# Optimization experiments

Hardware: AMD Instinct MI355X
Metric: run time of the kernel (lower is better)

## Reference

```python
import jax, jax.numpy as jnp
import numpy as np

B, S, D = 8, 2048, 512
DK, DV = 64, 64

def setup_inputs() -> dict:
    key = jax.random.key(0)
    ks = jax.random.split(key, 9)
    glorot = lambda k, shape: jax.random.uniform(k, shape, jnp.float32, -1.0, 1.0) * np.sqrt(6.0 / (shape[0] + shape[-1] if len(shape) > 1 else shape[0] + 1))
    return {
        "x_q": jax.random.normal(ks[0], (B, S, D), jnp.float32),
        "x_k": jax.random.normal(ks[1], (B, S, D), jnp.float32),
        "x_v": jax.random.normal(ks[2], (B, S, D), jnp.float32),
        "Wq": glorot(ks[3], (D, DK)), "bq": glorot(ks[4], (DK,)),
        "Wk": glorot(ks[5], (D, DK)), "bk": glorot(ks[6], (DK,)),
        "Wv": glorot(ks[7], (D, DV)), "bv": glorot(ks[8], (DV,)),
    }

def reference(x_q, x_k, x_v, Wq, bq, Wk, bk, Wv, bv):
    q = jnp.einsum("bsd,dk->bsk", x_q, Wq) + bq          # [B,S,DK]
    k = jnp.einsum("bsd,dk->bsk", x_k, Wk) + bk          # [B,S,DK]
    v = jnp.einsum("bsd,dv->bsv", x_v, Wv) + bv          # [B,S,DV]
    scale = 1.0 / np.sqrt(DK).astype(np.float32)
    scores = jnp.einsum("bqk,bsk->bqs", q, k) * scale     # [B,S,S]
    attn = jax.nn.softmax(scores, axis=-1)
    return jnp.einsum("bqs,bsv->bqv", attn, v)            # [B,S,DV]
```

## Files before the change

kernel.cpp:

```cpp
#include <hip/hip_runtime.h>
#include <stdint.h>

typedef __bf16 bf16;
typedef __bf16 bf16x8 __attribute__((ext_vector_type(8)));
typedef float f32x4 __attribute__((ext_vector_type(4)));

struct alignas(8) U16x4 { uint16_t v[4]; };

__device__ __forceinline__ f32x4 mfma16(bf16x8 a, bf16x8 b, f32x4 c) {
    return __builtin_amdgcn_mfma_f32_16x16x32_bf16(a, b, c, 0, 0, 0);
}

__device__ __forceinline__ void gload_lds16(const void* g, void* l) {
    __builtin_amdgcn_global_load_lds(
        (const __attribute__((address_space(1))) uint32_t*)g,
        (__attribute__((address_space(3))) uint32_t*)l, 16, 0, 0);
}

__device__ __forceinline__ uint16_t bf_bits(bf16 v) {
    return __builtin_bit_cast(uint16_t, v);
}

__device__ __forceinline__ float bf2f(uint16_t u) {
    uint32_t x = (uint32_t)u << 16;
    return __builtin_bit_cast(float, x);
}

#define QSCALE 0.18033688011112042f

__global__ __launch_bounds__(256)
void wprep_kernel(const float* __restrict__ Wq, const float* __restrict__ Wk,
                  const float* __restrict__ Wv, uint16_t* __restrict__ wt)
{
    const int tid = blockIdx.x * 256 + threadIdx.x;
    const int p   = tid >> 12;
    const int rem = tid & 4095;
    const int kt  = rem >> 8;
    const int f   = (rem >> 6) & 3;
    const int l   = rem & 63;
    const int n   = (l & 15) + 16 * f;
    const int k0  = kt * 32 + (l >> 4) * 8;
    const float* W = (p == 0) ? Wq : (p == 1) ? Wk : Wv;
    bf16x8 v;
    #pragma unroll
    for (int j = 0; j < 8; j++)
        v[j] = (bf16)W[(size_t)(k0 + j) * 64 + n];
    *(bf16x8*)(wt + (size_t)tid * 8) = v;
}

__global__ __launch_bounds__(256, 2)
void proj_kernel(const float* __restrict__ xq, const float* __restrict__ xk,
                 const float* __restrict__ xv,
                 const float* __restrict__ bq, const float* __restrict__ bk,
                 const float* __restrict__ bv,
                 const uint16_t* __restrict__ wt,
                 uint16_t* __restrict__ q_ws, uint16_t* __restrict__ k_ws,
                 uint16_t* __restrict__ vt_ws)
{
    const int p = blockIdx.y;
    const float* x    = (p == 0) ? xq : (p == 1) ? xk : xv;
    const float* bias = (p == 0) ? bq : (p == 1) ? bk : bv;
    const uint16_t* wtp = wt + (size_t)p * 32768;

    const int m0 = blockIdx.x * 64;
    const int t  = threadIdx.x;
    const int l  = t & 63;
    const int w  = t >> 6;

    __shared__ __align__(16) uint16_t sW[32768];

    const int arow = m0 + w * 16 + (l & 15);
    const int kg   = (l >> 4) * 8;
    const float* xrow = x + (size_t)arow * 512 + kg;

    float4 av0[8], av1[8];
    #pragma unroll
    for (int s = 0; s < 8; s++) {
        av0[s] = *(const float4*)(xrow + s * 32);
        av1[s] = *(const float4*)(xrow + s * 32 + 4);
    }

    #pragma unroll
    for (int r = 0; r < 16; r++)
        gload_lds16(wtp + (size_t)(r * 256 + t) * 8, (char*)sW + (r * 256 + t) * 16);

    __syncthreads();

    f32x4 acc[4];
    const f32x4 zero = {0.f, 0.f, 0.f, 0.f};
    #pragma unroll
    for (int f = 0; f < 4; f++) acc[f] = zero;

    #pragma unroll
    for (int kt = 0; kt < 16; kt++) {
        const int slot = kt & 7;
        bf16x8 a;
        a[0] = (bf16)av0[slot].x; a[1] = (bf16)av0[slot].y;
        a[2] = (bf16)av0[slot].z; a[3] = (bf16)av0[slot].w;
        a[4] = (bf16)av1[slot].x; a[5] = (bf16)av1[slot].y;
        a[6] = (bf16)av1[slot].z; a[7] = (bf16)av1[slot].w;
        if (kt < 8) {
            const int kb = (kt + 8) * 32;
            av0[slot] = *(const float4*)(xrow + kb);
            av1[slot] = *(const float4*)(xrow + kb + 4);
        }
        #pragma unroll
        for (int f = 0; f < 4; f++) {
            bf16x8 bfr = *(const bf16x8*)((const char*)sW + ((kt * 4 + f) * 64 + l) * 16);
            acc[f] = mfma16(a, bfr, acc[f]);
        }
    }

    float bv4[4];
    #pragma unroll
    for (int f = 0; f < 4; f++) bv4[f] = bias[16 * f + (l & 15)];

    if (p < 2) {
        uint16_t* outp = (p == 0) ? q_ws : k_ws;
        const float scale = (p == 0) ? QSCALE : 1.0f;
        #pragma unroll
        for (int f = 0; f < 4; f++)
            #pragma unroll
            for (int r = 0; r < 4; r++) {
                const int row = m0 + w * 16 + (l >> 4) * 4 + r;
                const int col = 16 * f + (l & 15);
                outp[(size_t)row * 64 + col] = bf_bits((bf16)((acc[f][r] + bv4[f]) * scale));
            }
    } else {
        #pragma unroll
        for (int f = 0; f < 4; f++) {
            const int row0 = m0 + w * 16 + (l >> 4) * 4;
            const int col  = 16 * f + (l & 15);
            const int bb = row0 >> 11;
            const int s0 = row0 & 2047;
            U16x4 pk;
            #pragma unroll
            for (int r = 0; r < 4; r++)
                pk.v[r] = bf_bits((bf16)(acc[f][r] + bv4[f]));
            *(U16x4*)(vt_ws + ((size_t)bb * 64 + col) * 2048 + s0) = pk;
        }
    }
}

template <int NCHUNK>
__global__ __launch_bounds__(512, 4)
void attn_kernel(const uint16_t* __restrict__ q_ws, const uint16_t* __restrict__ k_ws,
                 const uint16_t* __restrict__ vt_ws, float* __restrict__ out,
                 uint16_t* __restrict__ O_part, float* __restrict__ m_arr,
                 float* __restrict__ l_arr)
{
    constexpr int NT = 32 / NCHUNK;
    const int qt = blockIdx.x, b = blockIdx.y, c = blockIdx.z;
    const int t = threadIdx.x, l = t & 63, w = t >> 6;
    const int q = l & 15, g = l >> 4;
    const int q0 = qt * 128;

    __shared__ __align__(16) uint16_t sK[2][64 * 64];
    __shared__ __align__(16) uint16_t sV[2][64 * 64];
    __shared__ __align__(16) uint16_t sP[8][16 * 64];

    const uint16_t* qp = q_ws + ((size_t)(b * 2048 + q0)) * 64;
    const uint16_t* kp = k_ws + (size_t)b * 2048 * 64;
    const uint16_t* vp = vt_ws + (size_t)b * 64 * 2048;

    bf16x8 aq[2];
    #pragma unroll
    for (int ks = 0; ks < 2; ks++)
        aq[ks] = *(const bf16x8*)(qp + (size_t)(w * 16 + q) * 64 + g * 8 + ks * 32);

    const f32x4 zero = {0.f, 0.f, 0.f, 0.f};
    f32x4 acco[4];
    #pragma unroll
    for (int f = 0; f < 4; f++) acco[f] = zero;
    float m_st = -__builtin_inff();
    float l_st = 0.f;

    auto stage = [&](int tile, int buf) {
        const int kv0  = tile * 64;
        const int row  = t >> 3;
        const int slot = (t & 7) ^ (row & 7);
        gload_lds16(kp + (size_t)(kv0 + row) * 64 + slot * 8,
                    (char*)sK[buf] + t * 16);
        gload_lds16(vp + (size_t)row * 2048 + kv0 + slot * 8,
                    (char*)sV[buf] + t * 16);
    };

    stage(c * NT, 0);
    __syncthreads();

    for (int i = 0; i < NT; i++) {
        const int buf = i & 1;
        if (i < NT - 1) stage(c * NT + i + 1, buf ^ 1);

        f32x4 accs[4];
        #pragma unroll
        for (int f = 0; f < 4; f++) accs[f] = zero;
        #pragma unroll
        for (int ks = 0; ks < 2; ks++) {
            const int kb = g * 16 + ks * 64;
            #pragma unroll
            for (int f = 0; f < 4; f++) {
                const int srow = q + 16 * f;
                bf16x8 bk = *(const bf16x8*)((const char*)sK[buf] + srow * 128 + (kb ^ ((srow & 7) << 4)));
                accs[f] = mfma16(bk, aq[ks], accs[f]);
            }
        }

        float mx = accs[0][0];
        #pragma unroll
        for (int f = 0; f < 4; f++)
            #pragma unroll
            for (int r = 0; r < 4; r++) mx = fmaxf(mx, accs[f][r]);
        mx = fmaxf(mx, __shfl_xor(mx, 16));
        mx = fmaxf(mx, __shfl_xor(mx, 32));

        const bool skip = __all(mx <= m_st);
        float corr = 1.f;
        if (!skip) {
            const float mnew = fmaxf(m_st, mx);
            corr = exp2f(m_st - mnew);
            m_st = mnew;
        }

        float rs = 0.f;
        #pragma unroll
        for (int f = 0; f < 4; f++) {
            U16x4 pk;
            #pragma unroll
            for (int r = 0; r < 4; r++) {
                const float pv = exp2f(accs[f][r] - m_st);
                rs += pv;
                pk.v[r] = bf_bits((bf16)pv);
            }
            const int byte = q * 128 + ((32 * f + 8 * g) ^ ((q & 7) << 4));
            *(U16x4*)((char*)sP[w] + byte) = pk;
        }
        rs += __shfl_xor(rs, 16);
        rs += __shfl_xor(rs, 32);

        if (!skip) {
            l_st = l_st * corr + rs;
            #pragma unroll
            for (int r = 0; r < 4; r++) {
                const float cb = __shfl(corr, (g * 4 + r) + (l & 48));
                #pragma unroll
                for (int f = 0; f < 4; f++) acco[f][r] *= cb;
            }
        } else {
            l_st += rs;
        }

        asm volatile("s_waitcnt lgkmcnt(0)" ::: "memory");

        #pragma unroll
        for (int ks = 0; ks < 2; ks++) {
            bf16x8 ap = *(const bf16x8*)((const char*)sP[w] + q * 128 + ((ks * 64 + g * 16) ^ ((q & 7) << 4)));
            const int kb = g * 16 + ks * 64;
            #pragma unroll
            for (int f = 0; f < 4; f++) {
                const int vrow = q + 16 * f;
                bf16x8 bv2 = *(const bf16x8*)((const char*)sV[buf] + vrow * 128 + (kb ^ ((vrow & 7) << 4)));
                acco[f] = mfma16(ap, bv2, acco[f]);
            }
        }
        __syncthreads();
    }

    if constexpr (NCHUNK == 1) {
        #pragma unroll
        for (int r = 0; r < 4; r++) {
            const float lb = __shfl(l_st, (g * 4 + r) + (l & 48));
            #pragma unroll
            for (int f = 0; f < 4; f++) {
                const int qrow = q0 + w * 16 + g * 4 + r;
                const int col  = 16 * f + q;
                out[((size_t)(b * 2048 + qrow)) * 64 + col] = acco[f][r] / lb;
            }
        }
    } else {
        #pragma unroll
        for (int f = 0; f < 4; f++)
            #pragma unroll
            for (int r = 0; r < 4; r++) {
                const int qrow = q0 + w * 16 + g * 4 + r;
                const int col  = 16 * f + q;
                O_part[((size_t)c * 16384 + b * 2048 + qrow) * 64 + col] =
                    bf_bits((bf16)acco[f][r]);
            }
        if (l < 16) {
            const size_t idx = (size_t)c * 16384 + b * 2048 + q0 + w * 16 + l;
            m_arr[idx] = m_st;
            l_arr[idx] = l_st;
        }
    }
}

__global__ __launch_bounds__(256, 8)
void combine_kernel(const uint16_t* __restrict__ O_part, const float* __restrict__ m_arr,
                    const float* __restrict__ l_arr, float* __restrict__ out)
{
    const int b = blockIdx.y;
    const int r0 = (blockIdx.x >> 2) * 64 + (blockIdx.x & 3) * 16;
    const int t = threadIdx.x;
    const int col = t & 63;
    const int rg = t >> 6;

    #pragma unroll
    for (int pass = 0; pass < 4; pass++) {
        const int qrow = r0 + pass * 4 + rg;
        const size_t ridx = (size_t)b * 2048 + qrow;
        float m[4], lv[4];
        #pragma unroll
        for (int c = 0; c < 4; c++) {
            m[c]  = m_arr[(size_t)c * 16384 + ridx];
            lv[c] = l_arr[(size_t)c * 16384 + ridx];
        }
        const float M = fmaxf(fmaxf(m[0], m[1]), fmaxf(m[2], m[3]));
        float L = 0.f, wgt[4];
        #pragma unroll
        for (int c = 0; c < 4; c++) { wgt[c] = exp2f(m[c] - M); L += lv[c] * wgt[c]; }
        float acc = 0.f;
        #pragma unroll
        for (int c = 0; c < 4; c++)
            acc += bf2f(O_part[((size_t)c * 16384 + ridx) * 64 + col]) * wgt[c];
        out[ridx * 64 + col] = acc / L;
    }
}

extern "C" void kernel_launch(void* const* d_in, const int* in_sizes, int n_in,
                              void* d_out, int out_size, void* d_ws, size_t ws_size,
                              hipStream_t stream) {
    const float* xq = (const float*)d_in[0];
    const float* xk = (const float*)d_in[1];
    const float* xv = (const float*)d_in[2];
    const float* Wq = (const float*)d_in[3];
    const float* bq = (const float*)d_in[4];
    const float* Wk = (const float*)d_in[5];
    const float* bk = (const float*)d_in[6];
    const float* Wv = (const float*)d_in[7];
    const float* bv = (const float*)d_in[8];

    uint16_t* q_ws  = (uint16_t*)d_ws;
    uint16_t* k_ws  = q_ws + (size_t)16384 * 64;
    uint16_t* vt_ws = k_ws + (size_t)16384 * 64;
    uint16_t* wt    = vt_ws + (size_t)16384 * 64;
    uint16_t* O_part = wt + (size_t)3 * 4096 * 8;
    float* m_arr  = (float*)(O_part + (size_t)4 * 16384 * 64);
    float* l_arr  = m_arr + (size_t)4 * 16384;
    float* out = (float*)d_out;

    const size_t need = (size_t)3 * 16384 * 64 * 2
                      + (size_t)3 * 4096 * 8 * 2
                      + (size_t)4 * 16384 * 64 * 2
                      + (size_t)2 * 4 * 16384 * 4;

    wprep_kernel<<<48, 256, 0, stream>>>(Wq, Wk, Wv, wt);
    proj_kernel<<<dim3(256, 3), 256, 0, stream>>>(xq, xk, xv, bq, bk, bv, wt,
                                                  q_ws, k_ws, vt_ws);
    if (ws_size >= need) {
        attn_kernel<4><<<dim3(16, 8, 4), 512, 0, stream>>>(q_ws, k_ws, vt_ws, out,
                                                           O_part, m_arr, l_arr);
        combine_kernel<<<dim3(128, 8), 256, 0, stream>>>(O_part, m_arr, l_arr, out);
    } else {
        attn_kernel<1><<<dim3(16, 8, 1), 512, 0, stream>>>(q_ws, k_ws, vt_ws, out,
                                                           nullptr, nullptr, nullptr);
    }
}
```

Baseline: 55.79 us.

## Fuse weight prep into projection and split-K combine into attention via atomic counter

Removes the separate weight-conversion kernel: each projection block now converts and transposes its own weight matrix from fp32 into shared memory. It also removes the combine kernel: the last attention chunk block to finish for a query tile, detected with an atomic counter, merges the partial outputs and writes the final result. The aim is to cut two kernel launches and their dependency gaps, at the cost of redundant weight conversion in every projection block and a fence plus atomic in the attention epilogue. The counters are reset inside the projection kernel so that each call starts from zero.

```diff
diff --git a/kernel.cpp b/kernel.cpp
--- a/kernel.cpp
+++ b/kernel.cpp
@@ -6,6 +6,7 @@
 typedef float f32x4 __attribute__((ext_vector_type(4)));
 
 struct alignas(8) U16x4 { uint16_t v[4]; };
+struct alignas(16) U16x8 { uint16_t v[8]; };
 
 __device__ __forceinline__ f32x4 mfma16(bf16x8 a, bf16x8 b, f32x4 c) {
     return __builtin_amdgcn_mfma_f32_16x16x32_bf16(a, b, c, 0, 0, 0);
@@ -28,39 +29,19 @@
 
 #define QSCALE 0.18033688011112042f
 
-__global__ __launch_bounds__(256)
-void wprep_kernel(const float* __restrict__ Wq, const float* __restrict__ Wk,
-                  const float* __restrict__ Wv, uint16_t* __restrict__ wt)
-{
-    const int tid = blockIdx.x * 256 + threadIdx.x;
-    const int p   = tid >> 12;
-    const int rem = tid & 4095;
-    const int kt  = rem >> 8;
-    const int f   = (rem >> 6) & 3;
-    const int l   = rem & 63;
-    const int n   = (l & 15) + 16 * f;
-    const int k0  = kt * 32 + (l >> 4) * 8;
-    const float* W = (p == 0) ? Wq : (p == 1) ? Wk : Wv;
-    bf16x8 v;
-    #pragma unroll
-    for (int j = 0; j < 8; j++)
-        v[j] = (bf16)W[(size_t)(k0 + j) * 64 + n];
-    *(bf16x8*)(wt + (size_t)tid * 8) = v;
-}
-
 __global__ __launch_bounds__(256, 2)
 void proj_kernel(const float* __restrict__ xq, const float* __restrict__ xk,
                  const float* __restrict__ xv,
-                 const float* __restrict__ bq, const float* __restrict__ bk,
-                 const float* __restrict__ bv,
-                 const uint16_t* __restrict__ wt,
+                 const float* __restrict__ Wq, const float* __restrict__ bq,
+                 const float* __restrict__ Wk, const float* __restrict__ bk,
+                 const float* __restrict__ Wv, const float* __restrict__ bv,
                  uint16_t* __restrict__ q_ws, uint16_t* __restrict__ k_ws,
-                 uint16_t* __restrict__ vt_ws)
+                 uint16_t* __restrict__ vt_ws, uint32_t* __restrict__ cnt)
 {
     const int p = blockIdx.y;
     const float* x    = (p == 0) ? xq : (p == 1) ? xk : xv;
+    const float* W    = (p == 0) ? Wq : (p == 1) ? Wk : Wv;
     const float* bias = (p == 0) ? bq : (p == 1) ? bk : bv;
-    const uint16_t* wtp = wt + (size_t)p * 32768;
 
     const int m0 = blockIdx.x * 64;
     const int t  = threadIdx.x;
@@ -69,6 +50,8 @@
 
     __shared__ __align__(16) uint16_t sW[32768];
 
+    if (blockIdx.x == 0 && p == 0 && t < 128) cnt[t] = 0;
+
     const int arow = m0 + w * 16 + (l & 15);
     const int kg   = (l >> 4) * 8;
     const float* xrow = x + (size_t)arow * 512 + kg;
@@ -80,9 +63,20 @@
         av1[s] = *(const float4*)(xrow + s * 32 + 4);
     }
 
-    #pragma unroll
-    for (int r = 0; r < 16; r++)
-        gload_lds16(wtp + (size_t)(r * 256 + t) * 8, (char*)sW + (r * 256 + t) * 16);
+    {
+        const int f2 = (t >> 6) & 3;
+        const int n  = (t & 15) + 16 * f2;
+        const int kq = ((t >> 4) & 3) * 8;
+        #pragma unroll 4
+        for (int r = 0; r < 16; r++) {
+            const int k0 = r * 32 + kq;
+            bf16x8 v;
+            #pragma unroll
+            for (int j = 0; j < 8; j++)
+                v[j] = (bf16)W[(size_t)(k0 + j) * 64 + n];
+            *(bf16x8*)((char*)sW + (r * 256 + t) * 16) = v;
+        }
+    }
 
     __syncthreads();
 
@@ -147,7 +141,7 @@
 void attn_kernel(const uint16_t* __restrict__ q_ws, const uint16_t* __restrict__ k_ws,
                  const uint16_t* __restrict__ vt_ws, float* __restrict__ out,
                  uint16_t* __restrict__ O_part, float* __restrict__ m_arr,
-                 float* __restrict__ l_arr)
+                 float* __restrict__ l_arr, uint32_t* __restrict__ cnt)
 {
     constexpr int NT = 32 / NCHUNK;
     const int qt = blockIdx.x, b = blockIdx.y, c = blockIdx.z;
@@ -158,6 +152,7 @@
     __shared__ __align__(16) uint16_t sK[2][64 * 64];
     __shared__ __align__(16) uint16_t sV[2][64 * 64];
     __shared__ __align__(16) uint16_t sP[8][16 * 64];
+    __shared__ uint32_t s_old;
 
     const uint16_t* qp = q_ws + ((size_t)(b * 2048 + q0)) * 64;
     const uint16_t* kp = k_ws + (size_t)b * 2048 * 64;
@@ -292,38 +287,58 @@
             m_arr[idx] = m_st;
             l_arr[idx] = l_st;
         }
-    }
-}
-
-__global__ __launch_bounds__(256, 8)
-void combine_kernel(const uint16_t* __restrict__ O_part, const float* __restrict__ m_arr,
-                    const float* __restrict__ l_arr, float* __restrict__ out)
-{
-    const int b = blockIdx.y;
-    const int r0 = (blockIdx.x >> 2) * 64 + (blockIdx.x & 3) * 16;
-    const int t = threadIdx.x;
-    const int col = t & 63;
-    const int rg = t >> 6;
-
-    #pragma unroll
-    for (int pass = 0; pass < 4; pass++) {
-        const int qrow = r0 + pass * 4 + rg;
-        const size_t ridx = (size_t)b * 2048 + qrow;
-        float m[4], lv[4];
-        #pragma unroll
-        for (int c = 0; c < 4; c++) {
-            m[c]  = m_arr[(size_t)c * 16384 + ridx];
-            lv[c] = l_arr[(size_t)c * 16384 + ridx];
-        }
-        const float M = fmaxf(fmaxf(m[0], m[1]), fmaxf(m[2], m[3]));
-        float L = 0.f, wgt[4];
-        #pragma unroll
-        for (int c = 0; c < 4; c++) { wgt[c] = exp2f(m[c] - M); L += lv[c] * wgt[c]; }
-        float acc = 0.f;
-        #pragma unroll
-        for (int c = 0; c < 4; c++)
-            acc += bf2f(O_part[((size_t)c * 16384 + ridx) * 64 + col]) * wgt[c];
-        out[ridx * 64 + col] = acc / L;
+
+        __threadfence();
+        if (t == 0)
+            s_old = __hip_atomic_fetch_add(&cnt[b * 16 + qt], 1u,
+                                           __ATOMIC_ACQ_REL, __HIP_MEMORY_SCOPE_AGENT);
+        __syncthreads();
+        if (s_old == NCHUNK - 1) {
+            __threadfence();
+            const int rl   = t >> 2;
+            const int coff = (t & 3) * 16;
+            const size_t ridx = (size_t)b * 2048 + q0 + rl;
+            float m[NCHUNK], lv[NCHUNK];
+            #pragma unroll
+            for (int c2 = 0; c2 < NCHUNK; c2++) {
+                m[c2]  = m_arr[(size_t)c2 * 16384 + ridx];
+                lv[c2] = l_arr[(size_t)c2 * 16384 + ridx];
+            }
+            float M = m[0];
+            #pragma unroll
+            for (int c2 = 1; c2 < NCHUNK; c2++) M = fmaxf(M, m[c2]);
+            float L = 0.f, wgt[NCHUNK];
+            #pragma unroll
+            for (int c2 = 0; c2 < NCHUNK; c2++) {
+                wgt[c2] = exp2f(m[c2] - M);
+                L += lv[c2] * wgt[c2];
+            }
+            float accv[16];
+            #pragma unroll
+            for (int j = 0; j < 16; j++) accv[j] = 0.f;
+            #pragma unroll
+            for (int c2 = 0; c2 < NCHUNK; c2++) {
+                const uint16_t* src = O_part + ((size_t)c2 * 16384 + ridx) * 64 + coff;
+                U16x8 a0 = *(const U16x8*)src;
+                U16x8 a1 = *(const U16x8*)(src + 8);
+                #pragma unroll
+                for (int j = 0; j < 8; j++) {
+                    accv[j]     += bf2f(a0.v[j]) * wgt[c2];
+                    accv[8 + j] += bf2f(a1.v[j]) * wgt[c2];
+                }
+            }
+            const float invL = 1.f / L;
+            float* dst = out + ridx * 64 + coff;
+            #pragma unroll
+            for (int j4 = 0; j4 < 4; j4++) {
+                float4 o;
+                o.x = accv[j4 * 4 + 0] * invL;
+                o.y = accv[j4 * 4 + 1] * invL;
+                o.z = accv[j4 * 4 + 2] * invL;
+                o.w = accv[j4 * 4 + 3] * invL;
+                *(float4*)(dst + j4 * 4) = o;
+            }
+        }
     }
 }
 
@@ -343,26 +358,24 @@
     uint16_t* q_ws  = (uint16_t*)d_ws;
     uint16_t* k_ws  = q_ws + (size_t)16384 * 64;
     uint16_t* vt_ws = k_ws + (size_t)16384 * 64;
-    uint16_t* wt    = vt_ws + (size_t)16384 * 64;
-    uint16_t* O_part = wt + (size_t)3 * 4096 * 8;
+    uint16_t* O_part = vt_ws + (size_t)16384 * 64;
     float* m_arr  = (float*)(O_part + (size_t)4 * 16384 * 64);
     float* l_arr  = m_arr + (size_t)4 * 16384;
+    uint32_t* cnt = (uint32_t*)(l_arr + (size_t)4 * 16384);
     float* out = (float*)d_out;
 
     const size_t need = (size_t)3 * 16384 * 64 * 2
-                      + (size_t)3 * 4096 * 8 * 2
                       + (size_t)4 * 16384 * 64 * 2
-                      + (size_t)2 * 4 * 16384 * 4;
-
-    wprep_kernel<<<48, 256, 0, stream>>>(Wq, Wk, Wv, wt);
-    proj_kernel<<<dim3(256, 3), 256, 0, stream>>>(xq, xk, xv, bq, bk, bv, wt,
-                                                  q_ws, k_ws, vt_ws);
+                      + (size_t)2 * 4 * 16384 * 4
+                      + 128 * 4;
+
+    proj_kernel<<<dim3(256, 3), 256, 0, stream>>>(xq, xk, xv, Wq, bq, Wk, bk, Wv, bv,
+                                                  q_ws, k_ws, vt_ws, cnt);
     if (ws_size >= need) {
         attn_kernel<4><<<dim3(16, 8, 4), 512, 0, stream>>>(q_ws, k_ws, vt_ws, out,
-                                                           O_part, m_arr, l_arr);
-        combine_kernel<<<dim3(128, 8), 256, 0, stream>>>(O_part, m_arr, l_arr, out);
+                                                           O_part, m_arr, l_arr, cnt);
     } else {
         attn_kernel<1><<<dim3(16, 8, 1), 512, 0, stream>>>(q_ws, k_ws, vt_ws, out,
-                                                           nullptr, nullptr, nullptr);
-    }
-}
+                                                           nullptr, nullptr, nullptr, nullptr);
+    }
+}
```

New measurement: 196.2 us. +251.7%, slower.
